# Kernel optimization log

Hardware: AMD Instinct MI355X
Metric: run time of the kernel (lower is better)

The kernel has to match this reference:

```python
import jax, jax.numpy as jnp
import numpy as np

D_MODEL = 1024
N_HEADS = 16
D_K = D_MODEL // N_HEADS
NEG = -1e9


def setup_inputs() -> dict:
    key = jax.random.key(0)
    ks = jax.random.split(key, 6)
    B, T, D = 4, 2048, D_MODEL
    s = 1.0 / np.sqrt(D)
    x = jax.random.normal(ks[0], (B, T, D), dtype=jnp.float32)
    Wq = jax.random.normal(ks[1], (D, D), dtype=jnp.float32) * s
    Wk = jax.random.normal(ks[2], (D, D), dtype=jnp.float32) * s
    Wv = jax.random.normal(ks[3], (D, D), dtype=jnp.float32) * s
    Wo = jax.random.normal(ks[4], (D, D), dtype=jnp.float32) * s
    bo = jnp.zeros((D,), dtype=jnp.float32)
    # causal mask: True above diagonal = masked (masked_fill where True)
    mask = jnp.triu(jnp.ones((T, T), dtype=bool), k=1)
    return {"x": x, "mask": mask, "Wq": Wq, "Wk": Wk, "Wv": Wv, "Wo": Wo, "bo": bo}


def reference(x, mask, Wq, Wk, Wv, Wo, bo):
    B, T, D = x.shape
    # torch nn.Linear: y = x @ W.T
    q = (x @ Wq.T).reshape(B, T, N_HEADS, D_K).transpose(0, 2, 1, 3)  # [B,H,T,dk]
    k = (x @ Wk.T).reshape(B, T, N_HEADS, D_K).transpose(0, 2, 1, 3)
    v = (x @ Wv.T).reshape(B, T, N_HEADS, D_K).transpose(0, 2, 1, 3)
    scores = jnp.einsum("bhqd,bhkd->bhqk", q, k) / np.sqrt(D_K)  # [B,H,T,T]
    scores = jnp.where(mask[:T, :T], NEG, scores)
    attn = jax.nn.softmax(scores, axis=-1)
    ctx = jnp.einsum("bhqk,bhkd->bhqd", attn, v)  # [B,H,T,dk]
    ctx = ctx.transpose(0, 2, 1, 3).reshape(B, T, D)
    return ctx @ Wo.T + bo
```

## Files before the change

### kernel.cpp

```cpp
#include <hip/hip_runtime.h>
#include <hip/hip_bf16.h>


typedef __attribute__((ext_vector_type(8))) short bf16x8;
typedef __attribute__((ext_vector_type(4))) float f32x4;

__device__ __forceinline__ unsigned short f2b(float x) {
  __hip_bfloat16 h = __float2bfloat16(x);
  return __builtin_bit_cast(unsigned short, h);
}

__device__ __forceinline__ void load_lds16(const void* g, void* l) {
  __builtin_amdgcn_global_load_lds((__attribute__((address_space(1))) void*)g,
                                   (__attribute__((address_space(3))) void*)l,
                                   16, 0, 0);
}

__global__ void cast_kernel(const float* __restrict__ x,
                            const float* __restrict__ w0, const float* __restrict__ w1,
                            const float* __restrict__ w2, const float* __restrict__ w3,
                            unsigned short* __restrict__ xb, unsigned short* __restrict__ wb) {
  int i = blockIdx.x * 256 + threadIdx.x;
  const float* src;
  unsigned short* dst;
  int c;
  if (i < 1048576) {
    src = x; dst = xb; c = i;
  } else {
    int cw = i - 1048576;
    int wi = cw >> 17;
    c = cw & 131071;
    src = (wi == 0) ? w0 : (wi == 1) ? w1 : (wi == 2) ? w2 : w3;
    dst = wb + ((size_t)wi << 20);
  }
  const float4* s4 = (const float4*)src;
  float4 a = s4[2 * c], b = s4[2 * c + 1];
  union { unsigned short u[8]; uint4 v; } r;
  r.u[0] = f2b(a.x); r.u[1] = f2b(a.y); r.u[2] = f2b(a.z); r.u[3] = f2b(a.w);
  r.u[4] = f2b(b.x); r.u[5] = f2b(b.y); r.u[6] = f2b(b.z); r.u[7] = f2b(b.w);
  ((uint4*)dst)[c] = r.v;
}

__launch_bounds__(512, 2)
__global__ void gemm_qkv(const unsigned short* __restrict__ A,
                         const unsigned short* __restrict__ Bw,
                         unsigned short* __restrict__ Cout) {
  __shared__ unsigned short At[3][256 * 64];
  __shared__ unsigned short Bt[3][128 * 64];

  const int tid = threadIdx.x;
  const int lane = tid & 63;
  const int w = tid >> 6;
  const int quad = lane >> 4;
  const int l15 = lane & 15;
  const int m0 = blockIdx.x * 256;
  const int n0 = blockIdx.y * 128;
  const int wm = (w & 3) * 64;
  const int wn = (w >> 2) * 64;
  const int sf = ((w >> 2) & 1) << 2;
  const int ss = 4 - sf;

  auto stageA = [&](int buf, int kt, int c) {
    int chunk = c * 512 + tid;
    int row = chunk >> 3;
    int scol = (chunk & 7) ^ (row & 7);
    load_lds16(A + (size_t)(m0 + row) * 1024 + kt + scol * 8,
               &At[buf][(c * 512 + (w << 6)) << 3]);
  };
  auto stageB = [&](int buf, int kt, int c) {
    int chunk = c * 512 + tid;
    int row = chunk >> 3;
    int scol = (chunk & 7) ^ (row & 7);
    load_lds16(Bw + (size_t)(n0 + row) * 1024 + kt + scol * 8,
               &Bt[buf][(c * 512 + (w << 6)) << 3]);
  };

  const f32x4 z4 = {0.f, 0.f, 0.f, 0.f};
  f32x4 acc[4][4];
#pragma unroll
  for (int i = 0; i < 4; ++i)
#pragma unroll
    for (int j = 0; j < 4; ++j) acc[i][j] = z4;

#pragma unroll
  for (int c = 0; c < 4; ++c) stageA(0, 0, c);
#pragma unroll
  for (int c = 0; c < 2; ++c) stageB(0, 0, c);
#pragma unroll
  for (int c = 0; c < 4; ++c) stageA(1, 64, c);
#pragma unroll
  for (int c = 0; c < 2; ++c) stageB(1, 64, c);
  asm volatile("s_waitcnt vmcnt(6)" ::: "memory");
  __builtin_amdgcn_s_barrier();
  __builtin_amdgcn_sched_barrier(0);

  int buf = 0;
  for (int t = 0; t < 16; ++t) {
    const int sbuf = (buf >= 1) ? buf - 1 : 2;
    const int skt = (t + 2) * 64;
    const bool st = (t < 14);

    bf16x8 aF[4], bF[4], aS[4], bS[4];

#pragma unroll
    for (int i = 0; i < 4; ++i) {
      int rowA = wm + i * 16 + l15;
      aF[i] = *(const bf16x8*)&At[buf][rowA * 64 + (((sf + quad) ^ (rowA & 7)) << 3)];
    }
#pragma unroll
    for (int j = 0; j < 4; ++j) {
      int rowB = wn + j * 16 + l15;
      bF[j] = *(const bf16x8*)&Bt[buf][rowB * 64 + (((sf + quad) ^ (rowB & 7)) << 3)];
    }
    if (st) { stageA(sbuf, skt, 0); stageA(sbuf, skt, 1); stageA(sbuf, skt, 2); }
#pragma unroll
    for (int i = 0; i < 4; ++i) {
      int rowA = wm + i * 16 + l15;
      aS[i] = *(const bf16x8*)&At[buf][rowA * 64 + (((ss + quad) ^ (rowA & 7)) << 3)];
    }
#pragma unroll
    for (int j = 0; j < 4; ++j) {
      int rowB = wn + j * 16 + l15;
      bS[j] = *(const bf16x8*)&Bt[buf][rowB * 64 + (((ss + quad) ^ (rowB & 7)) << 3)];
    }
    if (st) { stageA(sbuf, skt, 3); stageB(sbuf, skt, 0); stageB(sbuf, skt, 1); }

    __builtin_amdgcn_s_setprio(1);
#pragma unroll
    for (int i = 0; i < 4; ++i)
#pragma unroll
      for (int j = 0; j < 4; ++j)
        acc[i][j] = __builtin_amdgcn_mfma_f32_16x16x32_bf16(aF[i], bF[j], acc[i][j], 0, 0, 0);
#pragma unroll
    for (int i = 0; i < 4; ++i)
#pragma unroll
      for (int j = 0; j < 4; ++j)
        acc[i][j] = __builtin_amdgcn_mfma_f32_16x16x32_bf16(aS[i], bS[j], acc[i][j], 0, 0, 0);
    __builtin_amdgcn_s_setprio(0);

    if (t < 14) {
      asm volatile("s_waitcnt vmcnt(6)" ::: "memory");
    } else if (t == 14) {
      asm volatile("s_waitcnt vmcnt(0)" ::: "memory");
    }
    __builtin_amdgcn_s_barrier();
    __builtin_amdgcn_sched_barrier(0);

    buf = (buf < 2) ? buf + 1 : 0;
  }

  const int seg = n0 >> 10;
#pragma unroll
  for (int i = 0; i < 4; ++i) {
#pragma unroll
    for (int j = 0; j < 4; ++j) {
#pragma unroll
      for (int r = 0; r < 4; ++r) {
        int m = m0 + wm + i * 16 + quad * 4 + r;
        int n = n0 + wn + j * 16 + l15;
        int nn = n & 1023;
        float v = acc[i][j][r];
        if (seg == 0) {
          Cout[(size_t)m * 1024 + nn] = f2b(v);
        } else if (seg == 1) {
          (Cout + 8388608)[(size_t)m * 1024 + nn] = f2b(v);
        } else {
          int b = m >> 11, tq = m & 2047, hh = nn >> 6, d = nn & 63;
          (Cout + 16777216)[(((size_t)((b * 16 + hh) * 64 + d)) << 11) + tq] = f2b(v);
        }
      }
    }
  }
}

__launch_bounds__(512, 2)
__global__ void gemm_proj(const unsigned short* __restrict__ A,
                          const unsigned short* __restrict__ Bw,
                          const float* __restrict__ bias,
                          float* __restrict__ out) {
  __shared__ unsigned short At[3][256 * 64];
  __shared__ unsigned short Bt[3][128 * 64];

  const int tid = threadIdx.x;
  const int lane = tid & 63;
  const int w = tid >> 6;
  const int quad = lane >> 4;
  const int l15 = lane & 15;
  const int m0 = blockIdx.x * 256;
  const int n0 = blockIdx.y * 128;
  const int wm = (w & 3) * 64;
  const int wn = (w >> 2) * 64;
  const int sf = ((w >> 2) & 1) << 2;
  const int ss = 4 - sf;

  auto stageA = [&](int buf, int kt, int c) {
    int chunk = c * 512 + tid;
    int row = chunk >> 3;
    int scol = (chunk & 7) ^ (row & 7);
    load_lds16(A + (size_t)(m0 + row) * 1024 + kt + scol * 8,
               &At[buf][(c * 512 + (w << 6)) << 3]);
  };
  auto stageB = [&](int buf, int kt, int c) {
    int chunk = c * 512 + tid;
    int row = chunk >> 3;
    int scol = (chunk & 7) ^ (row & 7);
    load_lds16(Bw + (size_t)(n0 + row) * 1024 + kt + scol * 8,
               &Bt[buf][(c * 512 + (w << 6)) << 3]);
  };

  const f32x4 z4 = {0.f, 0.f, 0.f, 0.f};
  f32x4 acc[4][4];
#pragma unroll
  for (int i = 0; i < 4; ++i)
#pragma unroll
    for (int j = 0; j < 4; ++j) acc[i][j] = z4;

#pragma unroll
  for (int c = 0; c < 4; ++c) stageA(0, 0, c);
#pragma unroll
  for (int c = 0; c < 2; ++c) stageB(0, 0, c);
#pragma unroll
  for (int c = 0; c < 4; ++c) stageA(1, 64, c);
#pragma unroll
  for (int c = 0; c < 2; ++c) stageB(1, 64, c);
  asm volatile("s_waitcnt vmcnt(6)" ::: "memory");
  __builtin_amdgcn_s_barrier();
  __builtin_amdgcn_sched_barrier(0);

  int buf = 0;
  for (int t = 0; t < 16; ++t) {
    const int sbuf = (buf >= 1) ? buf - 1 : 2;
    const int skt = (t + 2) * 64;
    const bool st = (t < 14);

    bf16x8 aF[4], bF[4], aS[4], bS[4];

#pragma unroll
    for (int i = 0; i < 4; ++i) {
      int rowA = wm + i * 16 + l15;
      aF[i] = *(const bf16x8*)&At[buf][rowA * 64 + (((sf + quad) ^ (rowA & 7)) << 3)];
    }
#pragma unroll
    for (int j = 0; j < 4; ++j) {
      int rowB = wn + j * 16 + l15;
      bF[j] = *(const bf16x8*)&Bt[buf][rowB * 64 + (((sf + quad) ^ (rowB & 7)) << 3)];
    }
    if (st) { stageA(sbuf, skt, 0); stageA(sbuf, skt, 1); stageA(sbuf, skt, 2); }
#pragma unroll
    for (int i = 0; i < 4; ++i) {
      int rowA = wm + i * 16 + l15;
      aS[i] = *(const bf16x8*)&At[buf][rowA * 64 + (((ss + quad) ^ (rowA & 7)) << 3)];
    }
#pragma unroll
    for (int j = 0; j < 4; ++j) {
      int rowB = wn + j * 16 + l15;
      bS[j] = *(const bf16x8*)&Bt[buf][rowB * 64 + (((ss + quad) ^ (rowB & 7)) << 3)];
    }
    if (st) { stageA(sbuf, skt, 3); stageB(sbuf, skt, 0); stageB(sbuf, skt, 1); }

    __builtin_amdgcn_s_setprio(1);
#pragma unroll
    for (int i = 0; i < 4; ++i)
#pragma unroll
      for (int j = 0; j < 4; ++j)
        acc[i][j] = __builtin_amdgcn_mfma_f32_16x16x32_bf16(aF[i], bF[j], acc[i][j], 0, 0, 0);
#pragma unroll
    for (int i = 0; i < 4; ++i)
#pragma unroll
      for (int j = 0; j < 4; ++j)
        acc[i][j] = __builtin_amdgcn_mfma_f32_16x16x32_bf16(aS[i], bS[j], acc[i][j], 0, 0, 0);
    __builtin_amdgcn_s_setprio(0);

    if (t < 14) {
      asm volatile("s_waitcnt vmcnt(6)" ::: "memory");
    } else if (t == 14) {
      asm volatile("s_waitcnt vmcnt(0)" ::: "memory");
    }
    __builtin_amdgcn_s_barrier();
    __builtin_amdgcn_sched_barrier(0);

    buf = (buf < 2) ? buf + 1 : 0;
  }

#pragma unroll
  for (int i = 0; i < 4; ++i)
#pragma unroll
    for (int j = 0; j < 4; ++j) {
      int n = n0 + wn + j * 16 + l15;
      float bv = bias[n];
#pragma unroll
      for (int r = 0; r < 4; ++r) {
        int m = m0 + wm + i * 16 + quad * 4 + r;
        out[(size_t)m * 1024 + n] = acc[i][j][r] + bv;
      }
    }
}

__launch_bounds__(256, 3)
__global__ void attn_kernel(const unsigned short* __restrict__ Q,
                            const unsigned short* __restrict__ K,
                            const unsigned short* __restrict__ VT,
                            unsigned short* __restrict__ ctx) {
  __shared__ unsigned short Kt[2][64 * 64];
  __shared__ unsigned short Vt[2][64 * 64];
  __shared__ unsigned short Pt[128 * 64];

  const int tid = threadIdx.x;
  const int lane = tid & 63;
  const int w = tid >> 6;
  const int quad = lane >> 4;
  const int l15 = lane & 15;
  const int bh = blockIdx.x;
  const int qt = 15 - blockIdx.y;
  const int b = bh >> 4, h = bh & 15;

  const unsigned short* Kg = K + ((size_t)(b * 2048)) * 1024 + h * 64;
  const unsigned short* Vg = VT + ((size_t)bh * 64) * 2048;

  const float SC = 0.1803368801f;
  const float M0 = 11.0f;

  const int qb = qt * 128;
  const int jn = 2 * qt + 2;

  bf16x8 qa[2][2];
#pragma unroll
  for (int g = 0; g < 2; ++g) {
    const unsigned short* qbase =
        Q + ((size_t)(b * 2048 + qb + w * 32 + g * 16 + l15)) * 1024 + h * 64;
    qa[g][0] = *(const bf16x8*)(qbase + quad * 8);
    qa[g][1] = *(const bf16x8*)(qbase + 32 + quad * 8);
  }

  const f32x4 z4 = {0.f, 0.f, 0.f, 0.f};
  f32x4 o[2][4];
#pragma unroll
  for (int g = 0; g < 2; ++g)
#pragma unroll
    for (int nt = 0; nt < 4; ++nt) o[g][nt] = z4;
  float lrow[2] = {0.f, 0.f};

#pragma unroll
  for (int c = 0; c < 2; ++c) {
    int chunk = c * 256 + tid;
    int row = chunk >> 3;
    int scol = (chunk & 7) ^ (row & 7);
    load_lds16(Kg + (size_t)row * 1024 + scol * 8, &Kt[0][((c * 256 + (w << 6)) << 3)]);
    load_lds16(Vg + ((size_t)row << 11) + scol * 8, &Vt[0][((c * 256 + (w << 6)) << 3)]);
  }

  int cur = 0;
  for (int j = 0; j < jn; ++j) {
    const int j0 = j * 64;
    __syncthreads();

    if (j + 1 < jn) {
      const int nj0 = j0 + 64;
#pragma unroll
      for (int c = 0; c < 2; ++c) {
        int chunk = c * 256 + tid;
        int row = chunk >> 3;
        int scol = (chunk & 7) ^ (row & 7);
        load_lds16(Kg + (size_t)(nj0 + row) * 1024 + scol * 8,
                   &Kt[cur ^ 1][((c * 256 + (w << 6)) << 3)]);
        load_lds16(Vg + ((size_t)row << 11) + nj0 + scol * 8,
                   &Vt[cur ^ 1][((c * 256 + (w << 6)) << 3)]);
      }
    }

    f32x4 st[2][4];
#pragma unroll
    for (int g = 0; g < 2; ++g)
#pragma unroll
      for (int nt = 0; nt < 4; ++nt) st[g][nt] = z4;
#pragma unroll
    for (int ks = 0; ks < 2; ++ks) {
#pragma unroll
      for (int nt = 0; nt < 4; ++nt) {
        int rowK = nt * 16 + l15;
        bf16x8 kf = *(const bf16x8*)&Kt[cur][rowK * 64 + (((ks * 4 + quad) ^ (rowK & 7)) << 3)];
        st[0][nt] = __builtin_amdgcn_mfma_f32_16x16x32_bf16(kf, qa[0][ks], st[0][nt], 0, 0, 0);
        st[1][nt] = __builtin_amdgcn_mfma_f32_16x16x32_bf16(kf, qa[1][ks], st[1][nt], 0, 0, 0);
      }
    }

#pragma unroll
    for (int g = 0; g < 2; ++g) {
      const int qmin = qb + w * 32 + g * 16;
      const bool dg = (j0 + 63 > qmin);
      const int q = qmin + l15;
      float sum = 0.f;
#pragma unroll
      for (int nt = 0; nt < 4; ++nt) {
#pragma unroll
        for (int r = 0; r < 4; ++r) {
          float e = fmaf(st[g][nt][r], SC, -M0);
          if (dg) {
            int kpos = j0 + nt * 16 + quad * 4 + r;
            if (kpos > q) e = -1e30f;
          }
          float pv = __builtin_amdgcn_exp2f(e);
          st[g][nt][r] = pv;
          sum += pv;
        }
      }
      sum += __shfl_xor(sum, 16);
      sum += __shfl_xor(sum, 32);
      lrow[g] += sum;
    }

#pragma unroll
    for (int g = 0; g < 2; ++g) {
      const int qrow = w * 32 + g * 16 + l15;
#pragma unroll
      for (int nt = 0; nt < 4; ++nt) {
        ushort4 pk;
        pk.x = f2b(st[g][nt][0]); pk.y = f2b(st[g][nt][1]);
        pk.z = f2b(st[g][nt][2]); pk.w = f2b(st[g][nt][3]);
        int chunk = nt * 4 + quad;
        *(ushort4*)&Pt[qrow * 64 + ((chunk ^ l15) << 2)] = pk;
      }
    }

#pragma unroll
    for (int ks = 0; ks < 2; ++ks) {
      int c0 = ks * 8 + quad * 2;
      union { ushort4 hh[2]; bf16x8 v; } pu[2];
#pragma unroll
      for (int g = 0; g < 2; ++g) {
        const int qrow = w * 32 + g * 16 + l15;
        pu[g].hh[0] = *(const ushort4*)&Pt[qrow * 64 + ((c0 ^ l15) << 2)];
        pu[g].hh[1] = *(const ushort4*)&Pt[qrow * 64 + (((c0 + 1) ^ l15) << 2)];
      }
#pragma unroll
      for (int nt = 0; nt < 4; ++nt) {
        int rowV = nt * 16 + l15;
        bf16x8 vb = *(const bf16x8*)&Vt[cur][rowV * 64 + (((ks * 4 + quad) ^ (rowV & 7)) << 3)];
        o[0][nt] = __builtin_amdgcn_mfma_f32_16x16x32_bf16(pu[0].v, vb, o[0][nt], 0, 0, 0);
        o[1][nt] = __builtin_amdgcn_mfma_f32_16x16x32_bf16(pu[1].v, vb, o[1][nt], 0, 0, 0);
      }
    }
    cur ^= 1;
  }

#pragma unroll
  for (int g = 0; g < 2; ++g) {
    float lf[4];
#pragma unroll
    for (int r = 0; r < 4; ++r) lf[r] = 1.f / __shfl(lrow[g], quad * 4 + r);
#pragma unroll
    for (int nt = 0; nt < 4; ++nt) {
#pragma unroll
      for (int r = 0; r < 4; ++r) {
        int q = qb + w * 32 + g * 16 + quad * 4 + r;
        int dcol = nt * 16 + l15;
        ctx[((size_t)(b * 2048 + q)) * 1024 + h * 64 + dcol] = f2b(o[g][nt][r] * lf[r]);
      }
    }
  }
}

extern "C" void kernel_launch(void* const* d_in, const int* in_sizes, int n_in,
                              void* d_out, int out_size, void* d_ws, size_t ws_size,
                              hipStream_t stream) {
  const float* x  = (const float*)d_in[0];
  const float* Wq = (const float*)d_in[2];
  const float* Wk = (const float*)d_in[3];
  const float* Wv = (const float*)d_in[4];
  const float* Wo = (const float*)d_in[5];
  const float* bo = (const float*)d_in[6];
  float* out = (float*)d_out;

  unsigned short* xb  = (unsigned short*)d_ws;
  unsigned short* wb  = xb + 8388608;
  unsigned short* Qb  = wb + 4 * 1048576;
  unsigned short* Kb  = Qb + 8388608;
  unsigned short* VTb = Kb + 8388608;
  unsigned short* ctxb = xb;

  cast_kernel<<<6144, 256, 0, stream>>>(x, Wq, Wk, Wv, Wo, xb, wb);

  gemm_qkv<<<dim3(32, 24), 512, 0, stream>>>(xb, wb, Qb);

  attn_kernel<<<dim3(64, 16), 256, 0, stream>>>(Qb, Kb, VTb, ctxb);

  gemm_proj<<<dim3(32, 8), 512, 0, stream>>>(ctxb, wb + 3 * 1048576, bo, out);
}
```

Measured before the change: 252.7 us.

## Restructure QKV GEMM to 4 waves with 128x64 warp tiles and BK=32

The QKV projection GEMM now runs with 256 threads (4 waves) instead of 512, and each wave computes a 128x64 output tile (8x4 MFMA fragments) instead of 64x64. The K-step shrinks from 64 to 32 with a matching 4-chunk XOR swizzle, triple-buffered LDS, and 32 iterations. The aim is more register-level reuse of A/B fragments per LDS read and less LDS use per block. The cost is twice as many accumulator registers per thread and more barriers per unit of work, which may limit occupancy or latency hiding.

```diff
diff --git a/kernel.cpp b/kernel.cpp
--- a/kernel.cpp
+++ b/kernel.cpp
@@ -41,10 +41,127 @@
   ((uint4*)dst)[c] = r.v;
 }
 
-__launch_bounds__(512, 2)
+__launch_bounds__(256, 2)
 __global__ void gemm_qkv(const unsigned short* __restrict__ A,
                          const unsigned short* __restrict__ Bw,
                          unsigned short* __restrict__ Cout) {
+  __shared__ unsigned short At[3][256 * 32];
+  __shared__ unsigned short Bt[3][128 * 32];
+
+  const int tid = threadIdx.x;
+  const int lane = tid & 63;
+  const int w = tid >> 6;
+  const int quad = lane >> 4;
+  const int l15 = lane & 15;
+  const int m0 = blockIdx.x * 256;
+  const int n0 = blockIdx.y * 128;
+  const int wm = (w >> 1) * 128;
+  const int wn = (w & 1) * 64;
+
+  auto stageA = [&](int buf, int kt, int c) {
+    int chunk = c * 256 + tid;
+    int row = chunk >> 2;
+    int gc = (chunk & 3) ^ ((row >> 1) & 3);
+    load_lds16(A + (size_t)(m0 + row) * 1024 + kt + gc * 8,
+               &At[buf][(c * 256 + (w << 6)) << 3]);
+  };
+  auto stageB = [&](int buf, int kt, int c) {
+    int chunk = c * 256 + tid;
+    int row = chunk >> 2;
+    int gc = (chunk & 3) ^ ((row >> 1) & 3);
+    load_lds16(Bw + (size_t)(n0 + row) * 1024 + kt + gc * 8,
+               &Bt[buf][(c * 256 + (w << 6)) << 3]);
+  };
+
+  const f32x4 z4 = {0.f, 0.f, 0.f, 0.f};
+  f32x4 acc[8][4];
+#pragma unroll
+  for (int i = 0; i < 8; ++i)
+#pragma unroll
+    for (int j = 0; j < 4; ++j) acc[i][j] = z4;
+
+#pragma unroll
+  for (int c = 0; c < 4; ++c) stageA(0, 0, c);
+#pragma unroll
+  for (int c = 0; c < 2; ++c) stageB(0, 0, c);
+#pragma unroll
+  for (int c = 0; c < 4; ++c) stageA(1, 32, c);
+#pragma unroll
+  for (int c = 0; c < 2; ++c) stageB(1, 32, c);
+  asm volatile("s_waitcnt vmcnt(6)" ::: "memory");
+  __builtin_amdgcn_s_barrier();
+  __builtin_amdgcn_sched_barrier(0);
+
+  int buf = 0;
+  for (int t = 0; t < 32; ++t) {
+    const int sbuf = (buf >= 1) ? buf - 1 : 2;
+    const int skt = (t + 2) * 32;
+    const bool st = (t < 30);
+
+    bf16x8 af[8], bf[4];
+#pragma unroll
+    for (int i = 0; i < 8; ++i) {
+      int rowA = wm + i * 16 + l15;
+      af[i] = *(const bf16x8*)&At[buf][rowA * 32 + ((quad ^ ((rowA >> 1) & 3)) << 3)];
+    }
+#pragma unroll
+    for (int j = 0; j < 4; ++j) {
+      int rowB = wn + j * 16 + l15;
+      bf[j] = *(const bf16x8*)&Bt[buf][rowB * 32 + ((quad ^ ((rowB >> 1) & 3)) << 3)];
+    }
+    if (st) {
+      stageA(sbuf, skt, 0); stageA(sbuf, skt, 1);
+      stageA(sbuf, skt, 2); stageA(sbuf, skt, 3);
+      stageB(sbuf, skt, 0); stageB(sbuf, skt, 1);
+    }
+    __builtin_amdgcn_s_setprio(1);
+#pragma unroll
+    for (int i = 0; i < 8; ++i)
+#pragma unroll
+      for (int j = 0; j < 4; ++j)
+        acc[i][j] = __builtin_amdgcn_mfma_f32_16x16x32_bf16(af[i], bf[j], acc[i][j], 0, 0, 0);
+    __builtin_amdgcn_s_setprio(0);
+
+    if (t < 30) {
+      asm volatile("s_waitcnt vmcnt(6)" ::: "memory");
+    } else if (t == 30) {
+      asm volatile("s_waitcnt vmcnt(0)" ::: "memory");
+    }
+    __builtin_amdgcn_s_barrier();
+    __builtin_amdgcn_sched_barrier(0);
+
+    buf = (buf < 2) ? buf + 1 : 0;
+  }
+
+  const int seg = n0 >> 10;
+#pragma unroll
+  for (int i = 0; i < 8; ++i) {
+#pragma unroll
+    for (int j = 0; j < 4; ++j) {
+#pragma unroll
+      for (int r = 0; r < 4; ++r) {
+        int m = m0 + wm + i * 16 + quad * 4 + r;
+        int n = n0 + wn + j * 16 + l15;
+        int nn = n & 1023;
+        float v = acc[i][j][r];
+        if (seg == 0) {
+          Cout[(size_t)m * 1024 + nn] = f2b(v);
+        } else if (seg == 1) {
+          (Cout + 8388608)[(size_t)m * 1024 + nn] = f2b(v);
+        } else {
+          int b = m >> 11, tq = m & 2047, hh = nn >> 6, d = nn & 63;
+          (Cout + 16777216)[(((size_t)((b * 16 + hh) * 64 + d)) << 11) + tq] = f2b(v);
+        }
+      }
+    }
+  }
+}
+
+__launch_bounds__(512, 2)
+__global__ void gemm_proj(const unsigned short* __restrict__ A,
+                          const unsigned short* __restrict__ Bw,
+                          const float* __restrict__ bias,
+                          float* __restrict__ out) {
   __shared__ unsigned short At[3][256 * 64];
   __shared__ unsigned short Bt[3][128 * 64];
 
@@ -149,139 +266,6 @@
     buf = (buf < 2) ? buf + 1 : 0;
   }
 
-  const int seg = n0 >> 10;
-#pragma unroll
-  for (int i = 0; i < 4; ++i) {
-#pragma unroll
-    for (int j = 0; j < 4; ++j) {
-#pragma unroll
-      for (int r = 0; r < 4; ++r) {
-        int m = m0 + wm + i * 16 + quad * 4 + r;
-        int n = n0 + wn + j * 16 + l15;
-        int nn = n & 1023;
-        float v = acc[i][j][r];
-        if (seg == 0) {
-          Cout[(size_t)m * 1024 + nn] = f2b(v);
-        } else if (seg == 1) {
-          (Cout + 8388608)[(size_t)m * 1024 + nn] = f2b(v);
-        } else {
-          int b = m >> 11, tq = m & 2047, hh = nn >> 6, d = nn & 63;
-          (Cout + 16777216)[(((size_t)((b * 16 + hh) * 64 + d)) << 11) + tq] = f2b(v);
-        }
-      }
-    }
-  }
-}
-
-__launch_bounds__(512, 2)
-__global__ void gemm_proj(const unsigned short* __restrict__ A,
-                          const unsigned short* __restrict__ Bw,
-                          const float* __restrict__ bias,
-                          float* __restrict__ out) {
-  __shared__ unsigned short At[3][256 * 64];
-  __shared__ unsigned short Bt[3][128 * 64];
-
-  const int tid = threadIdx.x;
-  const int lane = tid & 63;
-  const int w = tid >> 6;
-  const int quad = lane >> 4;
-  const int l15 = lane & 15;
-  const int m0 = blockIdx.x * 256;
-  const int n0 = blockIdx.y * 128;
-  const int wm = (w & 3) * 64;
-  const int wn = (w >> 2) * 64;
-  const int sf = ((w >> 2) & 1) << 2;
-  const int ss = 4 - sf;
-
-  auto stageA = [&](int buf, int kt, int c) {
-    int chunk = c * 512 + tid;
-    int row = chunk >> 3;
-    int scol = (chunk & 7) ^ (row & 7);
-    load_lds16(A + (size_t)(m0 + row) * 1024 + kt + scol * 8,
-               &At[buf][(c * 512 + (w << 6)) << 3]);
-  };
-  auto stageB = [&](int buf, int kt, int c) {
-    int chunk = c * 512 + tid;
-    int row = chunk >> 3;
-    int scol = (chunk & 7) ^ (row & 7);
-    load_lds16(Bw + (size_t)(n0 + row) * 1024 + kt + scol * 8,
-               &Bt[buf][(c * 512 + (w << 6)) << 3]);
-  };
-
-  const f32x4 z4 = {0.f, 0.f, 0.f, 0.f};
-  f32x4 acc[4][4];
-#pragma unroll
-  for (int i = 0; i < 4; ++i)
-#pragma unroll
-    for (int j = 0; j < 4; ++j) acc[i][j] = z4;
-
-#pragma unroll
-  for (int c = 0; c < 4; ++c) stageA(0, 0, c);
-#pragma unroll
-  for (int c = 0; c < 2; ++c) stageB(0, 0, c);
-#pragma unroll
-  for (int c = 0; c < 4; ++c) stageA(1, 64, c);
-#pragma unroll
-  for (int c = 0; c < 2; ++c) stageB(1, 64, c);
-  asm volatile("s_waitcnt vmcnt(6)" ::: "memory");
-  __builtin_amdgcn_s_barrier();
-  __builtin_amdgcn_sched_barrier(0);
-
-  int buf = 0;
-  for (int t = 0; t < 16; ++t) {
-    const int sbuf = (buf >= 1) ? buf - 1 : 2;
-    const int skt = (t + 2) * 64;
-    const bool st = (t < 14);
-
-    bf16x8 aF[4], bF[4], aS[4], bS[4];
-
-#pragma unroll
-    for (int i = 0; i < 4; ++i) {
-      int rowA = wm + i * 16 + l15;
-      aF[i] = *(const bf16x8*)&At[buf][rowA * 64 + (((sf + quad) ^ (rowA & 7)) << 3)];
-    }
-#pragma unroll
-    for (int j = 0; j < 4; ++j) {
-      int rowB = wn + j * 16 + l15;
-      bF[j] = *(const bf16x8*)&Bt[buf][rowB * 64 + (((sf + quad) ^ (rowB & 7)) << 3)];
-    }
-    if (st) { stageA(sbuf, skt, 0); stageA(sbuf, skt, 1); stageA(sbuf, skt, 2); }
-#pragma unroll
-    for (int i = 0; i < 4; ++i) {
-      int rowA = wm + i * 16 + l15;
-      aS[i] = *(const bf16x8*)&At[buf][rowA * 64 + (((ss + quad) ^ (rowA & 7)) << 3)];
-    }
-#pragma unroll
-    for (int j = 0; j < 4; ++j) {
-      int rowB = wn + j * 16 + l15;
-      bS[j] = *(const bf16x8*)&Bt[buf][rowB * 64 + (((ss + quad) ^ (rowB & 7)) << 3)];
-    }
-    if (st) { stageA(sbuf, skt, 3); stageB(sbuf, skt, 0); stageB(sbuf, skt, 1); }
-
-    __builtin_amdgcn_s_setprio(1);
-#pragma unroll
-    for (int i = 0; i < 4; ++i)
-#pragma unroll
-      for (int j = 0; j < 4; ++j)
-        acc[i][j] = __builtin_amdgcn_mfma_f32_16x16x32_bf16(aF[i], bF[j], acc[i][j], 0, 0, 0);
-#pragma unroll
-    for (int i = 0; i < 4; ++i)
-#pragma unroll
-      for (int j = 0; j < 4; ++j)
-        acc[i][j] = __builtin_amdgcn_mfma_f32_16x16x32_bf16(aS[i], bS[j], acc[i][j], 0, 0, 0);
-    __builtin_amdgcn_s_setprio(0);
-
-    if (t < 14) {
-      asm volatile("s_waitcnt vmcnt(6)" ::: "memory");
-    } else if (t == 14) {
-      asm volatile("s_waitcnt vmcnt(0)" ::: "memory");
-    }
-    __builtin_amdgcn_s_barrier();
-    __builtin_amdgcn_sched_barrier(0);
-
-    buf = (buf < 2) ? buf + 1 : 0;
-  }
-
 #pragma unroll
   for (int i = 0; i < 4; ++i)
 #pragma unroll
@@ -480,7 +464,7 @@
 
   cast_kernel<<<6144, 256, 0, stream>>>(x, Wq, Wk, Wv, Wo, xb, wb);
 
-  gemm_qkv<<<dim3(32, 24), 512, 0, stream>>>(xb, wb, Qb);
+  gemm_qkv<<<dim3(32, 24), 256, 0, stream>>>(xb, wb, Qb);
 
   attn_kernel<<<dim3(64, 16), 256, 0, stream>>>(Qb, Kb, VTb, ctxb);
 
```

After: 259.6 us. 1.03x slower.

## Enlarge QKV GEMM tile to 256x256 with quadrant-split ping-pong pipeline

Applied to the files above, without the earlier changes.

The QKV projection GEMM now computes a 256x256 output tile per block, up from 256x128, halving the grid to 32x12. Each wave holds a 128x64 accumulator. The LDS is reorganised into two double-buffered slots split into 128-row halves, and each K-step is broken into four quadrant MFMA phases with interleaved LDS reads, staged global loads and barriers. The larger tile raises arithmetic intensity and cuts redundant A/B traffic, at the cost of doubled accumulator registers (which may hurt occupancy), more barriers, and fewer blocks, which could reduce CU utilisation.

```diff
diff --git a/kernel.cpp b/kernel.cpp
--- a/kernel.cpp
+++ b/kernel.cpp
@@ -45,6 +45,249 @@
 __global__ void gemm_qkv(const unsigned short* __restrict__ A,
                          const unsigned short* __restrict__ Bw,
                          unsigned short* __restrict__ Cout) {
+  __shared__ unsigned short At[2][2][128 * 64];
+  __shared__ unsigned short Bt[2][2][128 * 64];
+
+  const int tid = threadIdx.x;
+  const int lane = tid & 63;
+  const int w = tid >> 6;
+  const int quad = lane >> 4;
+  const int l15 = lane & 15;
+  const int m0 = blockIdx.x * 256;
+  const int n0 = blockIdx.y * 256;
+  const int wm = (w >> 2) * 128;
+  const int wn = (w & 3) * 64;
+
+  auto stA = [&](int slot, int hf, int tile, int c) {
+    int chunk = c * 512 + tid;
+    int row = chunk >> 3;
+    int scol = (chunk & 7) ^ (row & 7);
+    load_lds16(A + (size_t)(m0 + hf * 128 + row) * 1024 + tile * 64 + scol * 8,
+               &At[slot][hf][(c * 512 + (w << 6)) << 3]);
+  };
+  auto stB = [&](int slot, int hf, int tile, int c) {
+    int chunk = c * 512 + tid;
+    int row = chunk >> 3;
+    int scol = (chunk & 7) ^ (row & 7);
+    load_lds16(Bw + (size_t)(n0 + hf * 128 + row) * 1024 + tile * 64 + scol * 8,
+               &Bt[slot][hf][(c * 512 + (w << 6)) << 3]);
+  };
+  auto rdA = [&](int slot, int rA, int ks) -> bf16x8 {
+    int hf = rA >> 7, r = rA & 127;
+    return *(const bf16x8*)&At[slot][hf][r * 64 + (((ks * 4 + quad) ^ (r & 7)) << 3)];
+  };
+  auto rdB = [&](int slot, int rB, int ks) -> bf16x8 {
+    int hf = rB >> 7, r = rB & 127;
+    return *(const bf16x8*)&Bt[slot][hf][r * 64 + (((ks * 4 + quad) ^ (r & 7)) << 3)];
+  };
+
+  const f32x4 z4 = {0.f, 0.f, 0.f, 0.f};
+  f32x4 acc[8][4];
+#pragma unroll
+  for (int i = 0; i < 8; ++i)
+#pragma unroll
+    for (int j = 0; j < 4; ++j) acc[i][j] = z4;
+
+#pragma unroll
+  for (int c = 0; c < 2; ++c) { stA(0, 0, 0, c); stA(0, 1, 0, c); stB(0, 0, 0, c); stB(0, 1, 0, c); }
+#pragma unroll
+  for (int c = 0; c < 2; ++c) { stA(1, 0, 1, c); stA(1, 1, 1, c); stB(1, 0, 1, c); stB(1, 1, 1, c); }
+  asm volatile("s_waitcnt vmcnt(8)" ::: "memory");
+  __builtin_amdgcn_s_barrier();
+  __builtin_amdgcn_sched_barrier(0);
+
+  for (int it = 0; it < 8; ++it) {
+    const int o = 2 * it + 1, E = 2 * it + 2, O = 2 * it + 3;
+    const bool stg = (it < 7);
+    bf16x8 a0[4][2], a1[4][2], b0[2][2], b1[2][2];
+
+#pragma unroll
+    for (int i = 0; i < 4; ++i)
+#pragma unroll
+      for (int ks = 0; ks < 2; ++ks) a0[i][ks] = rdA(0, wm + i * 16 + l15, ks);
+#pragma unroll
+    for (int j = 0; j < 2; ++j)
+#pragma unroll
+      for (int ks = 0; ks < 2; ++ks) b0[j][ks] = rdB(0, wn + j * 16 + l15, ks);
+    if (it > 0) { stA(1, 1, o, 0); stA(1, 1, o, 1); }
+    __builtin_amdgcn_s_barrier();
+    asm volatile("s_waitcnt lgkmcnt(0)" ::: "memory");
+    __builtin_amdgcn_sched_barrier(0);
+    __builtin_amdgcn_s_setprio(1);
+#pragma unroll
+    for (int i = 0; i < 4; ++i)
+#pragma unroll
+      for (int j = 0; j < 2; ++j)
+#pragma unroll
+        for (int ks = 0; ks < 2; ++ks)
+          acc[i][j] = __builtin_amdgcn_mfma_f32_16x16x32_bf16(a0[i][ks], b0[j][ks], acc[i][j], 0, 0, 0);
+    __builtin_amdgcn_s_setprio(0);
+    __builtin_amdgcn_s_barrier();
+
+#pragma unroll
+    for (int j = 0; j < 2; ++j)
+#pragma unroll
+      for (int ks = 0; ks < 2; ++ks) b1[j][ks] = rdB(0, wn + 32 + j * 16 + l15, ks);
+    __builtin_amdgcn_s_barrier();
+    asm volatile("s_waitcnt lgkmcnt(0)" ::: "memory");
+    __builtin_amdgcn_sched_barrier(0);
+    __builtin_amdgcn_s_setprio(1);
+#pragma unroll
+    for (int i = 0; i < 4; ++i)
+#pragma unroll
+      for (int j = 0; j < 2; ++j)
+#pragma unroll
+        for (int ks = 0; ks < 2; ++ks)
+          acc[i][2 + j] = __builtin_amdgcn_mfma_f32_16x16x32_bf16(a0[i][ks], b1[j][ks], acc[i][2 + j], 0, 0, 0);
+    __builtin_amdgcn_s_setprio(0);
+    __builtin_amdgcn_s_barrier();
+
+#pragma unroll
+    for (int i = 0; i < 4; ++i)
+#pragma unroll
+      for (int ks = 0; ks < 2; ++ks) a1[i][ks] = rdA(0, wm + 64 + i * 16 + l15, ks);
+    if (stg) { stB(0, 0, E, 0); stB(0, 0, E, 1); }
+    __builtin_amdgcn_s_barrier();
+    asm volatile("s_waitcnt lgkmcnt(0)" ::: "memory");
+    __builtin_amdgcn_sched_barrier(0);
+    __builtin_amdgcn_s_setprio(1);
+#pragma unroll
+    for (int i = 0; i < 4; ++i)
+#pragma unroll
+      for (int j = 0; j < 2; ++j)
+#pragma unroll
+        for (int ks = 0; ks < 2; ++ks)
+          acc[4 + i][2 + j] = __builtin_amdgcn_mfma_f32_16x16x32_bf16(a1[i][ks], b1[j][ks], acc[4 + i][2 + j], 0, 0, 0);
+    __builtin_amdgcn_s_setprio(0);
+    __builtin_amdgcn_s_barrier();
+
+    if (stg) { stB(0, 1, E, 0); stB(0, 1, E, 1); }
+    __builtin_amdgcn_s_barrier();
+    __builtin_amdgcn_sched_barrier(0);
+    __builtin_amdgcn_s_setprio(1);
+#pragma unroll
+    for (int i = 0; i < 4; ++i)
+#pragma unroll
+      for (int j = 0; j < 2; ++j)
+#pragma unroll
+        for (int ks = 0; ks < 2; ++ks)
+          acc[4 + i][j] = __builtin_amdgcn_mfma_f32_16x16x32_bf16(a1[i][ks], b0[j][ks], acc[4 + i][j], 0, 0, 0);
+    __builtin_amdgcn_s_setprio(0);
+    if (it < 7) {
+      asm volatile("s_waitcnt vmcnt(4)" ::: "memory");
+    } else {
+      asm volatile("s_waitcnt vmcnt(0)" ::: "memory");
+    }
+    __builtin_amdgcn_s_barrier();
+    __builtin_amdgcn_sched_barrier(0);
+
+#pragma unroll
+    for (int i = 0; i < 4; ++i)
+#pragma unroll
+      for (int ks = 0; ks < 2; ++ks) a0[i][ks] = rdA(1, wm + i * 16 + l15, ks);
+#pragma unroll
+    for (int j = 0; j < 2; ++j)
+#pragma unroll
+      for (int ks = 0; ks < 2; ++ks) b0[j][ks] = rdB(1, wn + j * 16 + l15, ks);
+    if (stg) { stA(0, 0, E, 0); stA(0, 0, E, 1); }
+    __builtin_amdgcn_s_barrier();
+    asm volatile("s_waitcnt lgkmcnt(0)" ::: "memory");
+    __builtin_amdgcn_sched_barrier(0);
+    __builtin_amdgcn_s_setprio(1);
+#pragma unroll
+    for (int i = 0; i < 4; ++i)
+#pragma unroll
+      for (int j = 0; j < 2; ++j)
+#pragma unroll
+        for (int ks = 0; ks < 2; ++ks)
+          acc[i][j] = __builtin_amdgcn_mfma_f32_16x16x32_bf16(a0[i][ks], b0[j][ks], acc[i][j], 0, 0, 0);
+    __builtin_amdgcn_s_setprio(0);
+    __builtin_amdgcn_s_barrier();
+
+#pragma unroll
+    for (int j = 0; j < 2; ++j)
+#pragma unroll
+      for (int ks = 0; ks < 2; ++ks) b1[j][ks] = rdB(1, wn + 32 + j * 16 + l15, ks);
+    if (stg) { stA(0, 1, E, 0); stA(0, 1, E, 1); }
+    __builtin_amdgcn_s_barrier();
+    asm volatile("s_waitcnt lgkmcnt(0)" ::: "memory");
+    __builtin_amdgcn_sched_barrier(0);
+    __builtin_amdgcn_s_setprio(1);
+#pragma unroll
+    for (int i = 0; i < 4; ++i)
+#pragma unroll
+      for (int j = 0; j < 2; ++j)
+#pragma unroll
+        for (int ks = 0; ks < 2; ++ks)
+          acc[i][2 + j] = __builtin_amdgcn_mfma_f32_16x16x32_bf16(a0[i][ks], b1[j][ks], acc[i][2 + j], 0, 0, 0);
+    __builtin_amdgcn_s_setprio(0);
+    __builtin_amdgcn_s_barrier();
+
+#pragma unroll
+    for (int i = 0; i < 4; ++i)
+#pragma unroll
+      for (int ks = 0; ks < 2; ++ks) a1[i][ks] = rdA(1, wm + 64 + i * 16 + l15, ks);
+    if (stg) { stB(1, 0, O, 0); stB(1, 0, O, 1); }
+    __builtin_amdgcn_s_barrier();
+    asm volatile("s_waitcnt lgkmcnt(0)" ::: "memory");
+    __builtin_amdgcn_sched_barrier(0);
+    __builtin_amdgcn_s_setprio(1);
+#pragma unroll
+    for (int i = 0; i < 4; ++i)
+#pragma unroll
+      for (int j = 0; j < 2; ++j)
+#pragma unroll
+        for (int ks = 0; ks < 2; ++ks)
+          acc[4 + i][2 + j] = __builtin_amdgcn_mfma_f32_16x16x32_bf16(a1[i][ks], b1[j][ks], acc[4 + i][2 + j], 0, 0, 0);
+    __builtin_amdgcn_s_setprio(0);
+    __builtin_amdgcn_s_barrier();
+
+    if (stg) { stB(1, 1, O, 0); stB(1, 1, O, 1); stA(1, 0, O, 0); stA(1, 0, O, 1); }
+    __builtin_amdgcn_s_barrier();
+    __builtin_amdgcn_sched_barrier(0);
+    __builtin_amdgcn_s_setprio(1);
+#pragma unroll
+    for (int i = 0; i < 4; ++i)
+#pragma unroll
+      for (int j = 0; j < 2; ++j)
+#pragma unroll
+        for (int ks = 0; ks < 2; ++ks)
+          acc[4 + i][j] = __builtin_amdgcn_mfma_f32_16x16x32_bf16(a1[i][ks], b0[j][ks], acc[4 + i][j], 0, 0, 0);
+    __builtin_amdgcn_s_setprio(0);
+    if (it < 7) asm volatile("s_waitcnt vmcnt(6)" ::: "memory");
+    __builtin_amdgcn_s_barrier();
+    __builtin_amdgcn_sched_barrier(0);
+  }
+
+  const int seg = n0 >> 10;
+#pragma unroll
+  for (int i = 0; i < 8; ++i) {
+#pragma unroll
+    for (int j = 0; j < 4; ++j) {
+#pragma unroll
+      for (int r = 0; r < 4; ++r) {
+        int m = m0 + wm + i * 16 + quad * 4 + r;
+        int n = n0 + wn + j * 16 + l15;
+        int nn = n & 1023;
+        float v = acc[i][j][r];
+        if (seg == 0) {
+          Cout[(size_t)m * 1024 + nn] = f2b(v);
+        } else if (seg == 1) {
+          (Cout + 8388608)[(size_t)m * 1024 + nn] = f2b(v);
+        } else {
+          int b = m >> 11, tq = m & 2047, hh = nn >> 6, d = nn & 63;
+          (Cout + 16777216)[(((size_t)((b * 16 + hh) * 64 + d)) << 11) + tq] = f2b(v);
+        }
+      }
+    }
+  }
+}
+
+__launch_bounds__(512, 2)
+__global__ void gemm_proj(const unsigned short* __restrict__ A,
+                          const unsigned short* __restrict__ Bw,
+                          const float* __restrict__ bias,
+                          float* __restrict__ out) {
   __shared__ unsigned short At[3][256 * 64];
   __shared__ unsigned short Bt[3][128 * 64];
 
@@ -149,139 +392,6 @@
     buf = (buf < 2) ? buf + 1 : 0;
   }
 
-  const int seg = n0 >> 10;
-#pragma unroll
-  for (int i = 0; i < 4; ++i) {
-#pragma unroll
-    for (int j = 0; j < 4; ++j) {
-#pragma unroll
-      for (int r = 0; r < 4; ++r) {
-        int m = m0 + wm + i * 16 + quad * 4 + r;
-        int n = n0 + wn + j * 16 + l15;
-        int nn = n & 1023;
-        float v = acc[i][j][r];
-        if (seg == 0) {
-          Cout[(size_t)m * 1024 + nn] = f2b(v);
-        } else if (seg == 1) {
-          (Cout + 8388608)[(size_t)m * 1024 + nn] = f2b(v);
-        } else {
-          int b = m >> 11, tq = m & 2047, hh = nn >> 6, d = nn & 63;
-          (Cout + 16777216)[(((size_t)((b * 16 + hh) * 64 + d)) << 11) + tq] = f2b(v);
-        }
-      }
-    }
-  }
-}
-
-__launch_bounds__(512, 2)
-__global__ void gemm_proj(const unsigned short* __restrict__ A,
-                          const unsigned short* __restrict__ Bw,
-                          const float* __restrict__ bias,
-                          float* __restrict__ out) {
-  __shared__ unsigned short At[3][256 * 64];
-  __shared__ unsigned short Bt[3][128 * 64];
-
-  const int tid = threadIdx.x;
-  const int lane = tid & 63;
-  const int w = tid >> 6;
-  const int quad = lane >> 4;
-  const int l15 = lane & 15;
-  const int m0 = blockIdx.x * 256;
-  const int n0 = blockIdx.y * 128;
-  const int wm = (w & 3) * 64;
-  const int wn = (w >> 2) * 64;
-  const int sf = ((w >> 2) & 1) << 2;
-  const int ss = 4 - sf;
-
-  auto stageA = [&](int buf, int kt, int c) {
-    int chunk = c * 512 + tid;
-    int row = chunk >> 3;
-    int scol = (chunk & 7) ^ (row & 7);
-    load_lds16(A + (size_t)(m0 + row) * 1024 + kt + scol * 8,
-               &At[buf][(c * 512 + (w << 6)) << 3]);
-  };
-  auto stageB = [&](int buf, int kt, int c) {
-    int chunk = c * 512 + tid;
-    int row = chunk >> 3;
-    int scol = (chunk & 7) ^ (row & 7);
-    load_lds16(Bw + (size_t)(n0 + row) * 1024 + kt + scol * 8,
-               &Bt[buf][(c * 512 + (w << 6)) << 3]);
-  };
-
-  const f32x4 z4 = {0.f, 0.f, 0.f, 0.f};
-  f32x4 acc[4][4];
-#pragma unroll
-  for (int i = 0; i < 4; ++i)
-#pragma unroll
-    for (int j = 0; j < 4; ++j) acc[i][j] = z4;
-
-#pragma unroll
-  for (int c = 0; c < 4; ++c) stageA(0, 0, c);
-#pragma unroll
-  for (int c = 0; c < 2; ++c) stageB(0, 0, c);
-#pragma unroll
-  for (int c = 0; c < 4; ++c) stageA(1, 64, c);
-#pragma unroll
-  for (int c = 0; c < 2; ++c) stageB(1, 64, c);
-  asm volatile("s_waitcnt vmcnt(6)" ::: "memory");
-  __builtin_amdgcn_s_barrier();
-  __builtin_amdgcn_sched_barrier(0);
-
-  int buf = 0;
-  for (int t = 0; t < 16; ++t) {
-    const int sbuf = (buf >= 1) ? buf - 1 : 2;
-    const int skt = (t + 2) * 64;
-    const bool st = (t < 14);
-
-    bf16x8 aF[4], bF[4], aS[4], bS[4];
-
-#pragma unroll
-    for (int i = 0; i < 4; ++i) {
-      int rowA = wm + i * 16 + l15;
-      aF[i] = *(const bf16x8*)&At[buf][rowA * 64 + (((sf + quad) ^ (rowA & 7)) << 3)];
-    }
-#pragma unroll
-    for (int j = 0; j < 4; ++j) {
-      int rowB = wn + j * 16 + l15;
-      bF[j] = *(const bf16x8*)&Bt[buf][rowB * 64 + (((sf + quad) ^ (rowB & 7)) << 3)];
-    }
-    if (st) { stageA(sbuf, skt, 0); stageA(sbuf, skt, 1); stageA(sbuf, skt, 2); }
-#pragma unroll
-    for (int i = 0; i < 4; ++i) {
-      int rowA = wm + i * 16 + l15;
-      aS[i] = *(const bf16x8*)&At[buf][rowA * 64 + (((ss + quad) ^ (rowA & 7)) << 3)];
-    }
-#pragma unroll
-    for (int j = 0; j < 4; ++j) {
-      int rowB = wn + j * 16 + l15;
-      bS[j] = *(const bf16x8*)&Bt[buf][rowB * 64 + (((ss + quad) ^ (rowB & 7)) << 3)];
-    }
-    if (st) { stageA(sbuf, skt, 3); stageB(sbuf, skt, 0); stageB(sbuf, skt, 1); }
-
-    __builtin_amdgcn_s_setprio(1);
-#pragma unroll
-    for (int i = 0; i < 4; ++i)
-#pragma unroll
-      for (int j = 0; j < 4; ++j)
-        acc[i][j] = __builtin_amdgcn_mfma_f32_16x16x32_bf16(aF[i], bF[j], acc[i][j], 0, 0, 0);
-#pragma unroll
-    for (int i = 0; i < 4; ++i)
-#pragma unroll
-      for (int j = 0; j < 4; ++j)
-        acc[i][j] = __builtin_amdgcn_mfma_f32_16x16x32_bf16(aS[i], bS[j], acc[i][j], 0, 0, 0);
-    __builtin_amdgcn_s_setprio(0);
-
-    if (t < 14) {
-      asm volatile("s_waitcnt vmcnt(6)" ::: "memory");
-    } else if (t == 14) {
-      asm volatile("s_waitcnt vmcnt(0)" ::: "memory");
-    }
-    __builtin_amdgcn_s_barrier();
-    __builtin_amdgcn_sched_barrier(0);
-
-    buf = (buf < 2) ? buf + 1 : 0;
-  }
-
 #pragma unroll
   for (int i = 0; i < 4; ++i)
 #pragma unroll
@@ -480,7 +590,7 @@
 
   cast_kernel<<<6144, 256, 0, stream>>>(x, Wq, Wk, Wv, Wo, xb, wb);
 
-  gemm_qkv<<<dim3(32, 24), 512, 0, stream>>>(xb, wb, Qb);
+  gemm_qkv<<<dim3(32, 12), 512, 0, stream>>>(xb, wb, Qb);
 
   attn_kernel<<<dim3(64, 16), 256, 0, stream>>>(Qb, Kb, VTb, ctxb);
 
```

After: 297.4 us. 17.7% more time.
